# Kernel tuning notes

Hardware: AMD Instinct MI355X
Metric: run time of the kernel (lower is better)

The kernel has to match this reference:

```python
import jax, jax.numpy as jnp
import numpy as np

STRIDES = (8, 16, 32, 64, 128)
TOPK = 1000          # fixed candidate count (jit-friendly stand-in for boolean masking)
SCORE_TH = 0.05      # from `score > 0.05` in postProcessing
IOU_TH = 0.5         # standard FCOS NMS threshold


def _decode_level(cls, cnt, reg, stride):
    # cls [B,C,H,W], cnt [B,1,H,W], reg [B,4,H,W]
    B, C, H, W = cls.shape
    p_cls = jax.nn.sigmoid(cls).transpose(0, 2, 3, 1).reshape(B, H * W, C)
    p_cnt = jax.nn.sigmoid(cnt).transpose(0, 2, 3, 1).reshape(B, H * W, 1)
    p_reg = jnp.exp(reg).transpose(0, 2, 3, 1).reshape(B, H * W, 4)  # (l,t,r,b) distances
    ys = (jnp.arange(H, dtype=cls.dtype) + 0.5) * stride
    xs = (jnp.arange(W, dtype=cls.dtype) + 0.5) * stride
    yy, xx = jnp.meshgrid(ys, xs, indexing='ij')
    cx = xx.reshape(-1)[None, :]  # [1,HW]
    cy = yy.reshape(-1)[None, :]
    boxes = jnp.stack([cx - p_reg[..., 0], cy - p_reg[..., 1],
                       cx + p_reg[..., 2], cy + p_reg[..., 3]], axis=-1)  # [B,HW,4]
    return p_cls, p_cnt, boxes


def _iou_matrix(b):
    # b [K,4] (x1,y1,x2,y2) -> [K,K]
    area = jnp.clip(b[:, 2] - b[:, 0], 0) * jnp.clip(b[:, 3] - b[:, 1], 0)
    x1 = jnp.maximum(b[:, None, 0], b[None, :, 0])
    y1 = jnp.maximum(b[:, None, 1], b[None, :, 1])
    x2 = jnp.minimum(b[:, None, 2], b[None, :, 2])
    y2 = jnp.minimum(b[:, None, 3], b[None, :, 3])
    inter = jnp.clip(x2 - x1, 0) * jnp.clip(y2 - y1, 0)
    return inter / (area[:, None] + area[None, :] - inter + 1e-9)


def _nms_keep(boxes, scores):
    # boxes [K,4] sorted by descending score, scores [K] -> keep mask [K]
    K = boxes.shape[0]
    iou = _iou_matrix(boxes)
    idx = jnp.arange(K)
    keep0 = scores > SCORE_TH
    def body(i, keep):
        sup = (iou[i] > IOU_TH) & (idx > i) & keep[i]
        return keep & ~sup
    return jax.lax.fori_loop(0, K, body, keep0)


def _detect(levels):
    cls_l, cnt_l, box_l = [], [], []
    for (c, n, r), s in zip(levels, STRIDES):
        pc, pn, pb = _decode_level(c, n, r, s)
        cls_l.append(pc); cnt_l.append(pn); box_l.append(pb)
    cls = jnp.concatenate(cls_l, 1)    # [B,N,C]
    boxes = jnp.concatenate(box_l, 1)  # [B,N,4]
    score = cls.max(-1)                # per original: score from cls (cnt unused in score)
    kind = cls.argmax(-1)
    top_s, top_i = jax.lax.top_k(score, TOPK)                      # [B,K]
    top_b = jnp.take_along_axis(boxes, top_i[..., None], axis=1)   # [B,K,4]
    top_k = jnp.take_along_axis(kind, top_i, axis=1)               # [B,K]
    keep = jax.vmap(_nms_keep)(top_b, top_s)                       # [B,K] bool
    out = jnp.concatenate([top_b,
                           top_k[..., None].astype(cls.dtype),
                           top_s[..., None],
                           keep[..., None].astype(cls.dtype)], axis=-1)  # [B,K,7]
    return out


def setup_inputs() -> dict:
    key = jax.random.key(0)
    B, C = 16, 20
    hw = [(128, 160), (64, 80), (32, 40), (16, 20), (8, 10)]
    names = []
    for p in (3, 4, 5, 6, 7):
        names += [f'cls_p{p}', f'cnt_p{p}', f'reg_p{p}']
    ks = jax.random.split(key, len(names))
    inp = {}
    for li, (H, W) in enumerate(hw):
        inp[f'cls_p{li+3}'] = jax.random.normal(ks[3*li+0], (B, C, H, W), jnp.float32)
        inp[f'cnt_p{li+3}'] = jax.random.normal(ks[3*li+1], (B, 1, H, W), jnp.float32)
        inp[f'reg_p{li+3}'] = jax.random.normal(ks[3*li+2], (B, 4, H, W), jnp.float32)
    return inp


def reference(cls_p3, cnt_p3, reg_p3, cls_p4, cnt_p4, reg_p4,
              cls_p5, cnt_p5, reg_p5, cls_p6, cnt_p6, reg_p6,
              cls_p7, cnt_p7, reg_p7):
    levels = [(cls_p3, cnt_p3, reg_p3), (cls_p4, cnt_p4, reg_p4),
              (cls_p5, cnt_p5, reg_p5), (cls_p6, cnt_p6, reg_p6),
              (cls_p7, cnt_p7, reg_p7)]
    return _detect(levels)
```

## Files before the change

kernel.cpp:

```cpp
#include <hip/hip_runtime.h>
#include <math.h>

#define BATCH 16
#define NCH 20
#define NPOS 27280
#define NTOP 1000
#define KW 16
#define NBIN 4096
#define CANDCAP 4096
#define NSLICE 14
#define SLICEPOS 2048

typedef unsigned long long u64;
typedef unsigned int u32;

__device__ __align__(16) u32 g_sb[BATCH * NPOS];
__device__ unsigned char g_kind[BATCH * NPOS];
__device__ u32 g_hph[BATCH * NSLICE * NBIN];
__device__ u32 g_suf[BATCH * NBIN];
__device__ u32 g_cnt[BATCH * NBIN];
__device__ u32 g_dcnt[BATCH * NBIN];
__device__ int g_ncand[BATCH];
__device__ u64 g_cand[BATCH * CANDCAP];
__device__ float4 g_box[BATCH * NTOP];
__device__ float g_score[BATCH * NTOP];
__device__ u64 g_maskT[BATCH * KW * NTOP];
__device__ unsigned char g_rowsup[BATCH * NTOP];

__device__ __forceinline__ int digit_of(u32 sb) {
  int d = ((int)sb - 0x3F000000) >> 11;
  return d < 0 ? 0 : (d > (NBIN - 1) ? (NBIN - 1) : d);
}

__device__ __forceinline__ int jj(int j) { return j + (j >> 6); }
#define SKEWCAP (NTOP + NTOP / 64 + 1)

__global__ __launch_bounds__(512) void k1_score(
    const float* __restrict__ c3, const float* __restrict__ c4,
    const float* __restrict__ c5, const float* __restrict__ c6,
    const float* __restrict__ c7) {
  int b = blockIdx.y, bx = blockIdx.x, tid = threadIdx.x;
  __shared__ u32 lh[NBIN];
  for (int j = tid; j < NBIN; j += 512) lh[j] = 0;
  int blkflat = b * NSLICE + bx;
  int z = blkflat * 512 + tid;
  if (z < BATCH * NBIN) g_dcnt[z] = 0;
  __syncthreads();

  int n0 = bx * SLICEPOS + tid * 4;
  if (n0 < NPOS) {
    const float* cls; int off, hw;
    if (n0 < 20480)      { cls = c3; off = 0;     hw = 20480; }
    else if (n0 < 25600) { cls = c4; off = 20480; hw = 5120;  }
    else if (n0 < 26880) { cls = c5; off = 25600; hw = 1280;  }
    else if (n0 < 27200) { cls = c6; off = 26880; hw = 320;   }
    else                 { cls = c7; off = 27200; hw = 80;    }
    int local = n0 - off;
    const float4* p = (const float4*)(cls + (size_t)b * NCH * hw + local);
    int s4 = hw >> 2;
    float4 best = p[0];
    int k0 = 0, k1 = 0, k2 = 0, k3 = 0;
    for (int c = 1; c < NCH; ++c) {
      float4 v = p[(size_t)c * s4];
      if (v.x > best.x) { best.x = v.x; k0 = c; }
      if (v.y > best.y) { best.y = v.y; k1 = c; }
      if (v.z > best.z) { best.z = v.z; k2 = c; }
      if (v.w > best.w) { best.w = v.w; k3 = c; }
    }
    float bb[4] = {best.x, best.y, best.z, best.w};
    u32 sb[4];
#pragma unroll
    for (int i = 0; i < 4; ++i) {
      float e = (float)exp(-(double)bb[i]);
      float s = 1.0f / (1.0f + e);
      sb[i] = __float_as_uint(s);
      atomicAdd(&lh[digit_of(sb[i])], 1u);
    }
    uint4 sb4; sb4.x = sb[0]; sb4.y = sb[1]; sb4.z = sb[2]; sb4.w = sb[3];
    *(uint4*)&g_sb[(size_t)b * NPOS + n0] = sb4;
    u32 kind4 = (u32)k0 | ((u32)k1 << 8) | ((u32)k2 << 16) | ((u32)k3 << 24);
    *(u32*)&g_kind[(size_t)b * NPOS + n0] = kind4;
  }
  __syncthreads();
  u32* ph = g_hph + ((size_t)b * NSLICE + bx) * NBIN;
  for (int j = tid; j < NBIN; j += 512) ph[j] = lh[j];
}

__global__ __launch_bounds__(1024) void k3_compact() {
  int b = blockIdx.y, bx = blockIdx.x, tid = threadIdx.x;
  int lane = tid & 63, wid = tid >> 6;
  __shared__ u32 suf[NBIN];
  __shared__ u32 wsum[16];
  __shared__ int sh_thr;

  u32 c[4];
#pragma unroll
  for (int k = 0; k < 4; ++k) {
    int d = 4 * tid + k;
    u32 s = 0;
    for (int p = 0; p < NSLICE; ++p) s += g_hph[((size_t)b * NSLICE + p) * NBIN + d];
    c[k] = s;
  }
  u32 tot = c[0] + c[1] + c[2] + c[3];
  u32 s = tot;
#pragma unroll
  for (int off = 1; off < 64; off <<= 1) {
    u32 v = __shfl_down(s, off);
    if (lane + off < 64) s += v;
  }
  if (lane == 0) wsum[wid] = s;
  __syncthreads();
  u32 wexcl = 0;
  for (int w2 = wid + 1; w2 < 16; ++w2) wexcl += wsum[w2];
  u32 e = wexcl + (s - tot);
  u32 e3 = e;
  u32 e2 = e3 + c[3];
  u32 e1 = e2 + c[2];
  u32 e0 = e1 + c[1];
  suf[4 * tid + 3] = e3;
  suf[4 * tid + 2] = e2;
  suf[4 * tid + 1] = e1;
  suf[4 * tid + 0] = e0;
  if (e3 < NTOP && NTOP <= e3 + c[3]) { sh_thr = 4 * tid + 3; if (bx == 0) g_ncand[b] = (int)(e3 + c[3]); }
  if (e2 < NTOP && NTOP <= e2 + c[2]) { sh_thr = 4 * tid + 2; if (bx == 0) g_ncand[b] = (int)(e2 + c[2]); }
  if (e1 < NTOP && NTOP <= e1 + c[1]) { sh_thr = 4 * tid + 1; if (bx == 0) g_ncand[b] = (int)(e1 + c[1]); }
  if (e0 < NTOP && NTOP <= e0 + c[0]) { sh_thr = 4 * tid + 0; if (bx == 0) g_ncand[b] = (int)(e0 + c[0]); }
  if (bx == 0) {
#pragma unroll
    for (int k = 0; k < 4; ++k) {
      g_cnt[b * NBIN + 4 * tid + k] = c[k];
    }
    g_suf[b * NBIN + 4 * tid + 0] = e0;
    g_suf[b * NBIN + 4 * tid + 1] = e1;
    g_suf[b * NBIN + 4 * tid + 2] = e2;
    g_suf[b * NBIN + 4 * tid + 3] = e3;
  }
  __syncthreads();
  int thr = sh_thr;

  int n0 = bx * SLICEPOS + tid * 2;
  if (n0 < NPOS) {
    uint2 sb2 = *(const uint2*)&g_sb[(size_t)b * NPOS + n0];
    u32 sb[2] = {sb2.x, sb2.y};
#pragma unroll
    for (int i = 0; i < 2; ++i) {
      int d = digit_of(sb[i]);
      if (d >= thr) {
        u32 slot = suf[d] + atomicAdd(&g_dcnt[b * NBIN + d], 1u);
        if (slot < CANDCAP)
          g_cand[b * CANDCAP + slot] = ((u64)sb[i] << 15) | (u32)(NPOS - (n0 + i));
      }
    }
  }
}

__global__ __launch_bounds__(256) void k4_rank(
    const float* __restrict__ r3, const float* __restrict__ r4,
    const float* __restrict__ r5, const float* __restrict__ r6,
    const float* __restrict__ r7, float* __restrict__ out) {
  int b = blockIdx.y, bx = blockIdx.x, tid = threadIdx.x;
  int ncand = g_ncand[b];
  if (ncand > CANDCAP) ncand = CANDCAP;
  for (int i = bx * 256 + tid; i < ncand; i += 8 * 256) {
    u64 k = g_cand[b * CANDCAP + i];
    int d = digit_of((u32)(k >> 15));
    u32 gs = g_suf[b * NBIN + d];
    u32 ge = gs + g_cnt[b * NBIN + d];
    if (ge > (u32)ncand) ge = (u32)ncand;
    int rank = (int)gs;
    for (u32 j = gs; j < ge; ++j) rank += (int)(g_cand[b * CANDCAP + j] > k);
    if (rank >= NTOP) continue;
    u32 n = (u32)NPOS - (u32)(k & 0x7FFFu);
    float sc = __uint_as_float((u32)(k >> 15));
    const float* reg; int off, hw, lvl;
    if (n < 20480)      { reg = r3; off = 0;     hw = 20480; lvl = 0; }
    else if (n < 25600) { reg = r4; off = 20480; hw = 5120;  lvl = 1; }
    else if (n < 26880) { reg = r5; off = 25600; hw = 1280;  lvl = 2; }
    else if (n < 27200) { reg = r6; off = 26880; hw = 320;   lvl = 3; }
    else                { reg = r7; off = 27200; hw = 80;    lvl = 4; }
    int local = (int)n - off;
    int W = 160 >> lvl;
    int hh = local / W, ww = local - hh * W;
    float stride = (float)(8 << lvl);
    const float* rp = reg + (size_t)b * 4 * hw + local;
    float e0 = expf(rp[0]);
    float e1 = expf(rp[(size_t)hw]);
    float e2 = expf(rp[(size_t)2 * hw]);
    float e3 = expf(rp[(size_t)3 * hw]);
    float cx = (ww + 0.5f) * stride, cy = (hh + 0.5f) * stride;
    float x1 = cx - e0, y1 = cy - e1, x2 = cx + e2, y2 = cy + e3;
    int ok = b * NTOP + rank;
    g_box[ok] = make_float4(x1, y1, x2, y2);
    g_score[ok] = sc;
    float* o = out + (size_t)ok * 7;
    o[0] = x1; o[1] = y1; o[2] = x2; o[3] = y2;
    o[4] = (float)g_kind[(size_t)b * NPOS + n];
    o[5] = sc;
  }
}

__global__ __launch_bounds__(256) void k5_mask() {
  int b = blockIdx.y;
  int ig = blockIdx.x;
  int tid = threadIdx.x;
  int lane = tid & 63;
  int jlo = ig * 16;
  int nst = NTOP - jlo;
  __shared__ float4 shbox[SKEWCAP];
  __shared__ float shA[SKEWCAP];
  const float4* boxes = g_box + b * NTOP;
  for (int j = tid; j < nst; j += 256) {
    float4 bj = boxes[jlo + j];
    shbox[jj(j)] = bj;
    shA[jj(j)] = fmaxf(bj.z - bj.x, 0.f) * fmaxf(bj.w - bj.y, 0.f);
  }
  __syncthreads();
  int i = jlo + (tid >> 4);
  int t = tid & 15;
  u64 word = 0;
  if (i < NTOP) {
    float4 bi = shbox[jj(i - jlo)];
    float aarea = shA[jj(i - jlo)];
    int j0 = t * 64;
    int jbeg = (j0 > i + 1) ? j0 : i + 1;
    int jend = (j0 + 64 < NTOP) ? j0 + 64 : NTOP;
    for (int j = jbeg; j < jend; ++j) {
      float4 bj = shbox[jj(j - jlo)];
      float barea = shA[jj(j - jlo)];
      float ix1 = fmaxf(bi.x, bj.x), iy1 = fmaxf(bi.y, bj.y);
      float ix2 = fminf(bi.z, bj.z), iy2 = fminf(bi.w, bj.w);
      float inter = fmaxf(ix2 - ix1, 0.f) * fmaxf(iy2 - iy1, 0.f);
      if (inter + inter > aarea + barea - inter + 1e-9f)
        word |= 1ull << (j - j0);
    }
    g_maskT[((size_t)b * KW + t) * NTOP + i] = word;
  }
  u64 b16 = __ballot(word != 0);
  int rg = lane >> 4;
  if (t == 0 && i < NTOP)
    g_rowsup[b * NTOP + i] = (unsigned char)(((b16 >> (rg * 16)) & 0xFFFFull) ? 1 : 0);
}

__global__ __launch_bounds__(64) void k6_greedy(float* __restrict__ out) {
  int b = blockIdx.x;
  int lane = threadIdx.x;
  int col = lane & 15, g = lane >> 4;
  const u64* maskT = g_maskT + (size_t)b * KW * NTOP;

  u64 mdiag[KW];
  float s[KW];
  unsigned char rs[KW];
#pragma unroll
  for (int w = 0; w < KW; ++w) {
    int k = w * 64 + lane;
    mdiag[w] = (k < NTOP) ? maskT[(size_t)w * NTOP + k] : 0ull;
    s[w] = (k < NTOP) ? g_score[b * NTOP + k] : 0.f;
    rs[w] = (k < NTOP) ? g_rowsup[b * NTOP + k] : (unsigned char)0;
  }

  u64 remv = 0;
  for (int w = 0; w < KW; ++w) {
    int k = w * 64 + lane;
    u64 keep0 = __ballot(k < NTOP && s[w] > 0.05f);
    u64 gate = __ballot(rs[w] != 0);
    u64 cur = keep0 & ~__shfl(remv, w);
    u64 rem = cur & gate;
    u64 acc = 0;
    while (rem) {
      int i = __ffsll(rem) - 1;
      u64 v = __shfl(mdiag[w], i);
      rem &= ~(v | (1ull << i));
      cur &= ~v;
      acc |= (1ull << i);
    }
    u64 upd = 0;
#pragma unroll
    for (int r = 0; r < 16; ++r) {
      int i2 = g * 16 + r;
      if ((acc >> i2) & 1ull) {
        int row = w * 64 + i2;
        if (row < NTOP) upd |= maskT[(size_t)col * NTOP + row];
      }
    }
    upd |= __shfl_xor(upd, 16);
    upd |= __shfl_xor(upd, 32);
    remv |= upd;
    if (k < NTOP) out[(size_t)(b * NTOP + k) * 7 + 6] = (float)((cur >> lane) & 1ull);
  }
}

extern "C" void kernel_launch(void* const* d_in, const int* in_sizes, int n_in,
                              void* d_out, int out_size, void* d_ws, size_t ws_size,
                              hipStream_t stream) {
  const float* c3 = (const float*)d_in[0];
  const float* r3 = (const float*)d_in[2];
  const float* c4 = (const float*)d_in[3];
  const float* r4 = (const float*)d_in[5];
  const float* c5 = (const float*)d_in[6];
  const float* r5 = (const float*)d_in[8];
  const float* c6 = (const float*)d_in[9];
  const float* r6 = (const float*)d_in[11];
  const float* c7 = (const float*)d_in[12];
  const float* r7 = (const float*)d_in[14];
  float* out = (float*)d_out;

  hipLaunchKernelGGL(k1_score, dim3(NSLICE, BATCH), dim3(512), 0, stream,
                     c3, c4, c5, c6, c7);
  hipLaunchKernelGGL(k3_compact, dim3(NSLICE, BATCH), dim3(1024), 0, stream);
  hipLaunchKernelGGL(k4_rank, dim3(8, BATCH), dim3(256), 0, stream,
                     r3, r4, r5, r6, r7, out);
  hipLaunchKernelGGL(k5_mask, dim3(63, BATCH), dim3(256), 0, stream);
  hipLaunchKernelGGL(k6_greedy, dim3(BATCH), dim3(64), 0, stream, out);
}
```

Measured before the change: 60.53 us.

## Fuse compact+rank and mask+greedy kernels via last-block-done atomic counters

Merges the compaction and rank kernels, and the mask and greedy-NMS kernels, so the pipeline launches three kernels instead of five. Each fused kernel uses a per-batch atomic completion counter, and the last finishing block runs the follow-on stage; the rank stage reads prefix sums from shared memory instead of global arrays. This removes launch gaps and some global traffic. In exchange, the rank stage now runs on one block per batch instead of eight, and the tail work is serialized behind the last arriving block.

Measured after the change: 228.3 us. +277.2%, slower.

```diff
diff --git a/kernel.cpp b/kernel.cpp
--- a/kernel.cpp
+++ b/kernel.cpp
@@ -17,15 +17,14 @@
 __device__ __align__(16) u32 g_sb[BATCH * NPOS];
 __device__ unsigned char g_kind[BATCH * NPOS];
 __device__ u32 g_hph[BATCH * NSLICE * NBIN];
-__device__ u32 g_suf[BATCH * NBIN];
-__device__ u32 g_cnt[BATCH * NBIN];
 __device__ u32 g_dcnt[BATCH * NBIN];
-__device__ int g_ncand[BATCH];
 __device__ u64 g_cand[BATCH * CANDCAP];
 __device__ float4 g_box[BATCH * NTOP];
 __device__ float g_score[BATCH * NTOP];
 __device__ u64 g_maskT[BATCH * KW * NTOP];
 __device__ unsigned char g_rowsup[BATCH * NTOP];
+__device__ int g_done1[BATCH];
+__device__ int g_done2[BATCH];
 
 __device__ __forceinline__ int digit_of(u32 sb) {
   int d = ((int)sb - 0x3F000000) >> 11;
@@ -45,6 +44,7 @@
   int blkflat = b * NSLICE + bx;
   int z = blkflat * 512 + tid;
   if (z < BATCH * NBIN) g_dcnt[z] = 0;
+  if (blkflat == 0 && tid < BATCH) { g_done1[tid] = 0; g_done2[tid] = 0; }
   __syncthreads();
 
   int n0 = bx * SLICEPOS + tid * 4;
@@ -86,12 +86,15 @@
   for (int j = tid; j < NBIN; j += 512) ph[j] = lh[j];
 }
 
-__global__ __launch_bounds__(1024) void k3_compact() {
+__global__ __launch_bounds__(1024) void k34_compact_rank(
+    const float* __restrict__ r3, const float* __restrict__ r4,
+    const float* __restrict__ r5, const float* __restrict__ r6,
+    const float* __restrict__ r7, float* __restrict__ out) {
   int b = blockIdx.y, bx = blockIdx.x, tid = threadIdx.x;
   int lane = tid & 63, wid = tid >> 6;
   __shared__ u32 suf[NBIN];
   __shared__ u32 wsum[16];
-  __shared__ int sh_thr;
+  __shared__ int sh_thr, sh_ncand, sh_last;
 
   u32 c[4];
 #pragma unroll
@@ -121,22 +124,13 @@
   suf[4 * tid + 2] = e2;
   suf[4 * tid + 1] = e1;
   suf[4 * tid + 0] = e0;
-  if (e3 < NTOP && NTOP <= e3 + c[3]) { sh_thr = 4 * tid + 3; if (bx == 0) g_ncand[b] = (int)(e3 + c[3]); }
-  if (e2 < NTOP && NTOP <= e2 + c[2]) { sh_thr = 4 * tid + 2; if (bx == 0) g_ncand[b] = (int)(e2 + c[2]); }
-  if (e1 < NTOP && NTOP <= e1 + c[1]) { sh_thr = 4 * tid + 1; if (bx == 0) g_ncand[b] = (int)(e1 + c[1]); }
-  if (e0 < NTOP && NTOP <= e0 + c[0]) { sh_thr = 4 * tid + 0; if (bx == 0) g_ncand[b] = (int)(e0 + c[0]); }
-  if (bx == 0) {
-#pragma unroll
-    for (int k = 0; k < 4; ++k) {
-      g_cnt[b * NBIN + 4 * tid + k] = c[k];
-    }
-    g_suf[b * NBIN + 4 * tid + 0] = e0;
-    g_suf[b * NBIN + 4 * tid + 1] = e1;
-    g_suf[b * NBIN + 4 * tid + 2] = e2;
-    g_suf[b * NBIN + 4 * tid + 3] = e3;
-  }
+  if (e3 < NTOP && NTOP <= e3 + c[3]) { sh_thr = 4 * tid + 3; sh_ncand = (int)(e3 + c[3]); }
+  if (e2 < NTOP && NTOP <= e2 + c[2]) { sh_thr = 4 * tid + 2; sh_ncand = (int)(e2 + c[2]); }
+  if (e1 < NTOP && NTOP <= e1 + c[1]) { sh_thr = 4 * tid + 1; sh_ncand = (int)(e1 + c[1]); }
+  if (e0 < NTOP && NTOP <= e0 + c[0]) { sh_thr = 4 * tid + 0; sh_ncand = (int)(e0 + c[0]); }
   __syncthreads();
   int thr = sh_thr;
+  int ncand = sh_ncand < CANDCAP ? sh_ncand : CANDCAP;
 
   int n0 = bx * SLICEPOS + tid * 2;
   if (n0 < NPOS) {
@@ -152,20 +146,18 @@
       }
     }
   }
-}
-
-__global__ __launch_bounds__(256) void k4_rank(
-    const float* __restrict__ r3, const float* __restrict__ r4,
-    const float* __restrict__ r5, const float* __restrict__ r6,
-    const float* __restrict__ r7, float* __restrict__ out) {
-  int b = blockIdx.y, bx = blockIdx.x, tid = threadIdx.x;
-  int ncand = g_ncand[b];
-  if (ncand > CANDCAP) ncand = CANDCAP;
-  for (int i = bx * 256 + tid; i < ncand; i += 8 * 256) {
+
+  __threadfence();
+  if (tid == 0) sh_last = (atomicAdd(&g_done1[b], 1) == NSLICE - 1) ? 1 : 0;
+  __syncthreads();
+  if (!sh_last) return;
+  __threadfence();
+
+  for (int i = tid; i < ncand; i += 1024) {
     u64 k = g_cand[b * CANDCAP + i];
     int d = digit_of((u32)(k >> 15));
-    u32 gs = g_suf[b * NBIN + d];
-    u32 ge = gs + g_cnt[b * NBIN + d];
+    u32 gs = suf[d];
+    u32 ge = (d > 0) ? suf[d - 1] : (u32)NPOS;
     if (ge > (u32)ncand) ge = (u32)ncand;
     int rank = (int)gs;
     for (u32 j = gs; j < ge; ++j) rank += (int)(g_cand[b * CANDCAP + j] > k);
@@ -199,7 +191,7 @@
   }
 }
 
-__global__ __launch_bounds__(256) void k5_mask() {
+__global__ __launch_bounds__(256) void k56_mask_greedy(float* __restrict__ out) {
   int b = blockIdx.y;
   int ig = blockIdx.x;
   int tid = threadIdx.x;
@@ -208,6 +200,7 @@
   int nst = NTOP - jlo;
   __shared__ float4 shbox[SKEWCAP];
   __shared__ float shA[SKEWCAP];
+  __shared__ int sh_last;
   const float4* boxes = g_box + b * NTOP;
   for (int j = tid; j < nst; j += 256) {
     float4 bj = boxes[jlo + j];
@@ -239,53 +232,57 @@
   int rg = lane >> 4;
   if (t == 0 && i < NTOP)
     g_rowsup[b * NTOP + i] = (unsigned char)(((b16 >> (rg * 16)) & 0xFFFFull) ? 1 : 0);
-}
-
-__global__ __launch_bounds__(64) void k6_greedy(float* __restrict__ out) {
-  int b = blockIdx.x;
-  int lane = threadIdx.x;
-  int col = lane & 15, g = lane >> 4;
-  const u64* maskT = g_maskT + (size_t)b * KW * NTOP;
-
-  u64 mdiag[KW];
-  float s[KW];
-  unsigned char rs[KW];
-#pragma unroll
-  for (int w = 0; w < KW; ++w) {
-    int k = w * 64 + lane;
-    mdiag[w] = (k < NTOP) ? maskT[(size_t)w * NTOP + k] : 0ull;
-    s[w] = (k < NTOP) ? g_score[b * NTOP + k] : 0.f;
-    rs[w] = (k < NTOP) ? g_rowsup[b * NTOP + k] : (unsigned char)0;
-  }
-
-  u64 remv = 0;
-  for (int w = 0; w < KW; ++w) {
-    int k = w * 64 + lane;
-    u64 keep0 = __ballot(k < NTOP && s[w] > 0.05f);
-    u64 gate = __ballot(rs[w] != 0);
-    u64 cur = keep0 & ~__shfl(remv, w);
-    u64 rem = cur & gate;
-    u64 acc = 0;
-    while (rem) {
-      int i = __ffsll(rem) - 1;
-      u64 v = __shfl(mdiag[w], i);
-      rem &= ~(v | (1ull << i));
-      cur &= ~v;
-      acc |= (1ull << i);
-    }
-    u64 upd = 0;
-#pragma unroll
-    for (int r = 0; r < 16; ++r) {
-      int i2 = g * 16 + r;
-      if ((acc >> i2) & 1ull) {
-        int row = w * 64 + i2;
-        if (row < NTOP) upd |= maskT[(size_t)col * NTOP + row];
+
+  __threadfence();
+  if (tid == 0) sh_last = (atomicAdd(&g_done2[b], 1) == 62) ? 1 : 0;
+  __syncthreads();
+  if (!sh_last) return;
+  __threadfence();
+
+  if (tid < 64) {
+    int col = lane & 15, g = lane >> 4;
+    const u64* maskT = g_maskT + (size_t)b * KW * NTOP;
+
+    u64 mdiag[KW];
+    float s[KW];
+    unsigned char rs[KW];
+#pragma unroll
+    for (int w = 0; w < KW; ++w) {
+      int k = w * 64 + lane;
+      mdiag[w] = (k < NTOP) ? maskT[(size_t)w * NTOP + k] : 0ull;
+      s[w] = (k < NTOP) ? g_score[b * NTOP + k] : 0.f;
+      rs[w] = (k < NTOP) ? g_rowsup[b * NTOP + k] : (unsigned char)0;
+    }
+
+    u64 remv = 0;
+    for (int w = 0; w < KW; ++w) {
+      int k = w * 64 + lane;
+      u64 keep0 = __ballot(k < NTOP && s[w] > 0.05f);
+      u64 gate = __ballot(rs[w] != 0);
+      u64 cur = keep0 & ~__shfl(remv, w);
+      u64 rem = cur & gate;
+      u64 acc = 0;
+      while (rem) {
+        int i2 = __ffsll(rem) - 1;
+        u64 v = __shfl(mdiag[w], i2);
+        rem &= ~(v | (1ull << i2));
+        cur &= ~v;
+        acc |= (1ull << i2);
       }
-    }
-    upd |= __shfl_xor(upd, 16);
-    upd |= __shfl_xor(upd, 32);
-    remv |= upd;
-    if (k < NTOP) out[(size_t)(b * NTOP + k) * 7 + 6] = (float)((cur >> lane) & 1ull);
+      u64 upd = 0;
+#pragma unroll
+      for (int r = 0; r < 16; ++r) {
+        int i2 = g * 16 + r;
+        if ((acc >> i2) & 1ull) {
+          int row = w * 64 + i2;
+          if (row < NTOP) upd |= maskT[(size_t)col * NTOP + row];
+        }
+      }
+      upd |= __shfl_xor(upd, 16);
+      upd |= __shfl_xor(upd, 32);
+      remv |= upd;
+      if (k < NTOP) out[(size_t)(b * NTOP + k) * 7 + 6] = (float)((cur >> lane) & 1ull);
+    }
   }
 }
 
@@ -306,9 +303,7 @@
 
   hipLaunchKernelGGL(k1_score, dim3(NSLICE, BATCH), dim3(512), 0, stream,
                      c3, c4, c5, c6, c7);
-  hipLaunchKernelGGL(k3_compact, dim3(NSLICE, BATCH), dim3(1024), 0, stream);
-  hipLaunchKernelGGL(k4_rank, dim3(8, BATCH), dim3(256), 0, stream,
+  hipLaunchKernelGGL(k34_compact_rank, dim3(NSLICE, BATCH), dim3(1024), 0, stream,
                      r3, r4, r5, r6, r7, out);
-  hipLaunchKernelGGL(k5_mask, dim3(63, BATCH), dim3(256), 0, stream);
-  hipLaunchKernelGGL(k6_greedy, dim3(BATCH), dim3(64), 0, stream, out);
-}
+  hipLaunchKernelGGL(k56_mask_greedy, dim3(63, BATCH), dim3(256), 0, stream, out);
+}
```
